# Kernel optimization log

Hardware: AMD Instinct MI355X
Metric: run time of the kernel (lower is better)

## Reference

```python
import jax, jax.numpy as jnp
import numpy as np

N, E, F_IN, HEADS, OUT_PER_HEAD = 50000, 1600000, 128, 4, 32
NEG_SLOPE = 0.2  # LeakyReLU slope used by standard GATConv


def setup_inputs() -> dict:
    key = jax.random.key(0)
    ks = jax.random.split(key, 7)
    x = jax.random.normal(ks[0], (N, F_IN), dtype=jnp.float32)
    edge_src = jax.random.randint(ks[1], (E,), 0, N, dtype=jnp.int64)
    edge_dst = jax.random.randint(ks[2], (E,), 0, N, dtype=jnp.int64)
    W = jax.random.normal(ks[3], (F_IN, HEADS * OUT_PER_HEAD), dtype=jnp.float32) / np.float32(np.sqrt(F_IN))
    a_src = jax.random.normal(ks[4], (HEADS, OUT_PER_HEAD), dtype=jnp.float32) * 0.1
    a_dst = jax.random.normal(ks[5], (HEADS, OUT_PER_HEAD), dtype=jnp.float32) * 0.1
    bias = jnp.zeros((HEADS * OUT_PER_HEAD,), dtype=jnp.float32)
    return {"x": x, "W": W, "a_src": a_src, "a_dst": a_dst, "bias": bias,
            "edge_src": edge_src, "edge_dst": edge_dst}


def reference(x, W, a_src, a_dst, bias, edge_src, edge_dst):
    # GATConv with concat=True over a static edge list (the faithful
    # static-shape form of tf.where(adj>0.5) -> gather -> GAT -> scatter).
    n = x.shape[0]
    H, D = a_src.shape
    h = (x @ W).reshape(n, H, D)                      # [N,H,D] projected features
    # per-node attention logits for source / destination roles
    e_s = jnp.einsum('nhd,hd->nh', h, a_src)          # [N,H]
    e_d = jnp.einsum('nhd,hd->nh', h, a_dst)          # [N,H]
    # per-edge logits with LeakyReLU
    e = jax.nn.leaky_relu(e_s[edge_src] + e_d[edge_dst], NEG_SLOPE)  # [E,H]
    # numerically stable softmax over incoming edges of each destination node
    m = jax.ops.segment_max(e, edge_dst, num_segments=n)             # [N,H]
    m = jnp.where(jnp.isfinite(m), m, 0.0)
    alpha = jnp.exp(e - m[edge_dst])                                 # [E,H]
    denom = jax.ops.segment_sum(alpha, edge_dst, num_segments=n)     # [N,H]
    alpha = alpha / jnp.where(denom > 0, denom, 1.0)[edge_dst]
    # weighted aggregation of source features onto destinations
    msgs = alpha[:, :, None] * h[edge_src]                           # [E,H,D]
    out = jax.ops.segment_sum(msgs, edge_dst, num_segments=n)        # [N,H,D]
    return out.reshape(n, H * D) + bias
```

## Files before the change

kernel.cpp:

```cpp
#include <hip/hip_runtime.h>
#include <math.h>

#define NEG_SLOPE 0.2f
#define NB1 256
#define XROW 136
#define BSHIFT 5
#define BNODES 32
#define CAP 2048

typedef __attribute__((ext_vector_type(8))) short short8;
typedef __attribute__((ext_vector_type(4))) float floatx4;

__device__ __forceinline__ unsigned short f2bf(float f) {
    unsigned int u = __float_as_uint(f);
    u += 0x7fffu + ((u >> 16) & 1u);
    return (unsigned short)(u >> 16);
}
__device__ __forceinline__ float bf2f(unsigned short b) {
    return __uint_as_float(((unsigned int)b) << 16);
}
__device__ __forceinline__ float u2fl(unsigned int u) {
    return __uint_as_float(u << 16);
}
__device__ __forceinline__ float u2fh(unsigned int u) {
    return __uint_as_float(u & 0xffff0000u);
}

__device__ __forceinline__ void fma8(float* a, int o, float wt, const uint4& hv) {
    a[o + 0] = fmaf(wt, u2fl(hv.x), a[o + 0]);
    a[o + 1] = fmaf(wt, u2fh(hv.x), a[o + 1]);
    a[o + 2] = fmaf(wt, u2fl(hv.y), a[o + 2]);
    a[o + 3] = fmaf(wt, u2fh(hv.y), a[o + 3]);
    a[o + 4] = fmaf(wt, u2fl(hv.z), a[o + 4]);
    a[o + 5] = fmaf(wt, u2fh(hv.z), a[o + 5]);
    a[o + 6] = fmaf(wt, u2fl(hv.w), a[o + 6]);
    a[o + 7] = fmaf(wt, u2fh(hv.w), a[o + 7]);
}

__global__ __launch_bounds__(256) void prep_w_kernel(
    const float* __restrict__ W, unsigned short* __restrict__ WThi,
    unsigned short* __restrict__ WTlo, int* __restrict__ gcur, int nbuck)
{
    const int idx = blockIdx.x * 256 + threadIdx.x;
    const int j = idx >> 7, k = idx & 127;
    const float w = W[k * 128 + j];
    const unsigned short hi = f2bf(w);
    const unsigned short lo = f2bf(w - bf2f(hi));
    WThi[idx] = hi;
    WTlo[idx] = lo;
    if (idx < nbuck) gcur[idx] = idx * CAP;
}

__global__ __launch_bounds__(256) void mfma_gemm_kernel(
    const float* __restrict__ x, const unsigned short* __restrict__ WThi,
    const unsigned short* __restrict__ WTlo, const float* __restrict__ a_src,
    const float* __restrict__ a_dst, unsigned short* __restrict__ hb,
    float* __restrict__ es, float* __restrict__ ed, int n)
{
    __shared__ unsigned short Xhi[32 * XROW];
    __shared__ unsigned short Xlo[32 * XROW];
    const int t = threadIdx.x;
    const int wv = t >> 6, lane = t & 63;
    const int l16 = lane & 15, quad = lane >> 4;
    const int node_base = blockIdx.x * 32;

    short8 bh[4][2], bl[4][2];
    #pragma unroll
    for (int c = 0; c < 4; ++c) {
        #pragma unroll
        for (int u = 0; u < 2; ++u) {
            const int j = (wv * 2 + u) * 16 + l16;
            const int ko = c * 32 + quad * 8;
            bh[c][u] = *(const short8*)&WThi[j * 128 + ko];
            bl[c][u] = *(const short8*)&WTlo[j * 128 + ko];
        }
    }

    for (int i = t; i < 1024; i += 256) {
        const int nd = i >> 5;
        const int k4 = i & 31;
        float4 xv = make_float4(0.f, 0.f, 0.f, 0.f);
        if (node_base + nd < n)
            xv = ((const float4*)(x + (size_t)(node_base + nd) * 128))[k4];
        const unsigned short h0 = f2bf(xv.x), h1 = f2bf(xv.y),
                             h2 = f2bf(xv.z), h3 = f2bf(xv.w);
        const unsigned short l0 = f2bf(xv.x - bf2f(h0)), l1 = f2bf(xv.y - bf2f(h1)),
                             l2 = f2bf(xv.z - bf2f(h2)), l3 = f2bf(xv.w - bf2f(h3));
        *(ushort4*)&Xhi[nd * XROW + k4 * 4] = make_ushort4(h0, h1, h2, h3);
        *(ushort4*)&Xlo[nd * XROW + k4 * 4] = make_ushort4(l0, l1, l2, l3);
    }
    __syncthreads();

    floatx4 acc[2][2] = {};
    #pragma unroll
    for (int c = 0; c < 4; ++c) {
        const int ko = c * 32 + quad * 8;
        short8 ah[2], al[2];
        #pragma unroll
        for (int r = 0; r < 2; ++r) {
            ah[r] = *(const short8*)&Xhi[(r * 16 + l16) * XROW + ko];
            al[r] = *(const short8*)&Xlo[(r * 16 + l16) * XROW + ko];
        }
        #pragma unroll
        for (int r = 0; r < 2; ++r)
        #pragma unroll
        for (int u = 0; u < 2; ++u) {
            acc[r][u] = __builtin_amdgcn_mfma_f32_16x16x32_bf16(ah[r], bl[c][u], acc[r][u], 0, 0, 0);
            acc[r][u] = __builtin_amdgcn_mfma_f32_16x16x32_bf16(al[r], bh[c][u], acc[r][u], 0, 0, 0);
            acc[r][u] = __builtin_amdgcn_mfma_f32_16x16x32_bf16(ah[r], bh[c][u], acc[r][u], 0, 0, 0);
        }
    }

    float asv[2], adv[2];
    #pragma unroll
    for (int u = 0; u < 2; ++u) {
        const int feat = (wv * 2 + u) * 16 + l16;
        asv[u] = a_src[feat];
        adv[u] = a_dst[feat];
    }
    #pragma unroll
    for (int r = 0; r < 2; ++r) {
        #pragma unroll
        for (int u = 0; u < 2; ++u) {
            const int feat = (wv * 2 + u) * 16 + l16;
            #pragma unroll
            for (int g = 0; g < 4; ++g) {
                const int node = node_base + r * 16 + quad * 4 + g;
                if (node < n)
                    hb[(size_t)node * 128 + feat] = f2bf(acc[r][u][g]);
            }
        }
        #pragma unroll
        for (int g = 0; g < 4; ++g) {
            float ps = acc[r][0][g] * asv[0] + acc[r][1][g] * asv[1];
            float pd = acc[r][0][g] * adv[0] + acc[r][1][g] * adv[1];
            #pragma unroll
            for (int o = 8; o >= 1; o >>= 1) {
                ps += __shfl_xor(ps, o);
                pd += __shfl_xor(pd, o);
            }
            const int node = node_base + r * 16 + quad * 4 + g;
            if (l16 == 0 && node < n) {
                es[node * 4 + wv] = ps;
                ed[node * 4 + wv] = pd;
            }
        }
    }
}

__global__ __launch_bounds__(256) void bucket_scatter(
    const int* __restrict__ src, const int* __restrict__ dst,
    int* __restrict__ gcur, int* __restrict__ ebuf, int e, int nbuck)
{
    __shared__ unsigned int stash[6272];
    __shared__ int cnt[1600];
    __shared__ int cur[1600];
    const int t = threadIdx.x;
    for (int b = t; b < nbuck; b += 256) cnt[b] = 0;
    __syncthreads();
    const int per = (e + NB1 - 1) / NB1;
    const int lo = blockIdx.x * per;
    const int m = min(e, lo + per) - lo;
    for (int j = t; j < m; j += 256) {
        const int d = dst[lo + j];
        const unsigned int v = (unsigned int)src[lo + j]
                             | ((unsigned int)(d & (BNODES - 1)) << 16)
                             | ((unsigned int)(d >> BSHIFT) << 21);
        stash[j] = v;
        atomicAdd(&cnt[d >> BSHIFT], 1);
    }
    __syncthreads();
    for (int b = t; b < nbuck; b += 256) {
        const int c = cnt[b];
        if (c > 0) cur[b] = atomicAdd(&gcur[b], c);
    }
    __syncthreads();
    for (int j = t; j < m; j += 256) {
        const unsigned int v = stash[j];
        const int pos = atomicAdd(&cur[v >> 21], 1);
        ebuf[pos] = (int)(v & 0x1FFFFFu);
    }
}

__global__ __launch_bounds__(256) void sort_agg_kernel(
    const unsigned short* __restrict__ hb, const float* __restrict__ es,
    const float* __restrict__ ed, const float* __restrict__ bias,
    const int* __restrict__ gcur, const int* __restrict__ ebuf,
    float* __restrict__ out, int n)
{
    __shared__ unsigned short esort[CAP];
    __shared__ int hist[BNODES], hexcl[BNODES], cur[BNODES];
    const int b = blockIdx.x;
    const int t = threadIdx.x;
    const int lane = t & 63;
    const int wv = t >> 6;
    const int l8 = lane & 7;
    const int oct = lane >> 3;
    const int f0 = l8 * 16;
    const int hh = l8 >> 1;

    const int start = b * CAP;
    const int end = gcur[b];

    if (t < BNODES) hist[t] = 0;
    __syncthreads();
    for (int i = start + t; i < end; i += 256)
        atomicAdd(&hist[(ebuf[i] >> 16) & (BNODES - 1)], 1);
    __syncthreads();
    if (wv == 0) {
        const int v = (lane < BNODES) ? hist[lane] : 0;
        int incl = v;
        #pragma unroll
        for (int o = 1; o < BNODES; o <<= 1) {
            const int tt = __shfl_up(incl, o);
            if (lane >= o) incl += tt;
        }
        if (lane < BNODES) { hexcl[lane] = incl - v; cur[lane] = incl - v; }
    }
    __syncthreads();
    for (int i = start + t; i < end; i += 256) {
        const int v = ebuf[i];
        const int pos = atomicAdd(&cur[(v >> 16) & (BNODES - 1)], 1);
        esort[pos] = (unsigned short)(v & 0xFFFF);
    }
    __syncthreads();

    for (int j = 0; j < 8; ++j) {
        const int nd = wv * 8 + j;
        const int node = b * BNODES + nd;
        if (node >= n) break;
        const int off = hexcl[nd];
        const int deg = hist[nd];
        const float edh = ed[(size_t)node * 4 + hh];

        float a[16];
        #pragma unroll
        for (int k = 0; k < 16; ++k) a[k] = 0.f;
        float wsum = 0.f;

        for (int c0 = 0; c0 < deg; c0 += 16) {
            const int ci0 = c0 + oct;
            const int ci1 = ci0 + 8;
            const int dm = deg - 1;
            const int s0 = esort[off + min(ci0, dm)];
            const int s1 = esort[off + min(ci1, dm)];
            const float e0 = es[(size_t)s0 * 4 + hh];
            const float e1 = es[(size_t)s1 * 4 + hh];
            const uint4 hA0 = *(const uint4*)&hb[(size_t)s0 * 128 + f0];
            const uint4 hB0 = *(const uint4*)&hb[(size_t)s0 * 128 + f0 + 8];
            const uint4 hA1 = *(const uint4*)&hb[(size_t)s1 * 128 + f0];
            const uint4 hB1 = *(const uint4*)&hb[(size_t)s1 * 128 + f0 + 8];
            float lg0 = e0 + edh; lg0 = lg0 > 0.f ? lg0 : NEG_SLOPE * lg0;
            float lg1 = e1 + edh; lg1 = lg1 > 0.f ? lg1 : NEG_SLOPE * lg1;
            const float w0 = (ci0 < deg) ? __expf(lg0) : 0.f;
            const float w1 = (ci1 < deg) ? __expf(lg1) : 0.f;
            fma8(a, 0, w0, hA0); fma8(a, 8, w0, hB0);
            fma8(a, 0, w1, hA1); fma8(a, 8, w1, hB1);
            wsum += w0 + w1;
        }
        #pragma unroll
        for (int o = 8; o <= 32; o <<= 1) {
            #pragma unroll
            for (int k = 0; k < 16; ++k) a[k] += __shfl_xor(a[k], o);
            wsum += __shfl_xor(wsum, o);
        }
        if (oct == 0) {
            const float inv = 1.f / ((wsum > 0.f) ? wsum : 1.f);
            #pragma unroll
            for (int q = 0; q < 4; ++q) {
                const float4 bq = *(const float4*)(bias + f0 + q * 4);
                float4 o4;
                o4.x = a[q * 4 + 0] * inv + bq.x;
                o4.y = a[q * 4 + 1] * inv + bq.y;
                o4.z = a[q * 4 + 2] * inv + bq.z;
                o4.w = a[q * 4 + 3] * inv + bq.w;
                *(float4*)(out + (size_t)node * 128 + f0 + q * 4) = o4;
            }
        }
    }
}

extern "C" void kernel_launch(void* const* d_in, const int* in_sizes, int n_in,
                              void* d_out, int out_size, void* d_ws, size_t ws_size,
                              hipStream_t stream)
{
    const float* x      = (const float*)d_in[0];
    const float* W      = (const float*)d_in[1];
    const float* a_src  = (const float*)d_in[2];
    const float* a_dst  = (const float*)d_in[3];
    const float* bias   = (const float*)d_in[4];
    const int*   e_src  = (const int*)d_in[5];
    const int*   e_dst  = (const int*)d_in[6];
    float* out = (float*)d_out;

    const int n = in_sizes[0] / 128;
    const int e = in_sizes[5];
    const int nbuck = (n + BNODES - 1) >> BSHIFT;

    char* ws = (char*)d_ws;
    size_t o = 0;
    auto alloc = [&](size_t bytes) { void* p = ws + o; o += (bytes + 255) & ~(size_t)255; return p; };
    unsigned short* hb   = (unsigned short*)alloc((size_t)n * 128 * sizeof(unsigned short));
    unsigned short* WThi = (unsigned short*)alloc(128 * 128 * sizeof(unsigned short));
    unsigned short* WTlo = (unsigned short*)alloc(128 * 128 * sizeof(unsigned short));
    float* es      = (float*)alloc((size_t)n * 4 * sizeof(float));
    float* ed      = (float*)alloc((size_t)n * 4 * sizeof(float));
    int* gcur      = (int*)alloc((size_t)nbuck * sizeof(int));
    int* ebuf      = (int*)alloc((size_t)nbuck * CAP * sizeof(int));
    (void)ws_size; (void)n_in; (void)out_size;

    prep_w_kernel<<<64, 256, 0, stream>>>(W, WThi, WTlo, gcur, nbuck);
    mfma_gemm_kernel<<<(n + 31) / 32, 256, 0, stream>>>(x, WThi, WTlo, a_src, a_dst,
                                                        hb, es, ed, n);
    bucket_scatter<<<NB1, 256, 0, stream>>>(e_src, e_dst, gcur, ebuf, e, nbuck);
    sort_agg_kernel<<<nbuck, 256, 0, stream>>>(hb, es, ed, bias, gcur, ebuf, out, n);
}
```

Before: 197.3 us.

## Use coarse 128-node buckets in scatter and unroll aggregation loop by 32

The edge bucketing pass now groups edges by 128-node coarse buckets, giving about 391 buckets instead of about 1563. This reduces per-block global atomics and makes ebuf writes less scattered. Each aggregation block then reads its whole coarse bucket and keeps only the quarter that belongs to its 32 fine nodes, so every coarse bucket is read four times. The gather loop is also unrolled to four edges per octet to put more memory loads in flight, at the cost of more registers and extra wasted lanes on low-degree nodes.

```diff
diff --git a/kernel.cpp b/kernel.cpp
--- a/kernel.cpp
+++ b/kernel.cpp
@@ -4,9 +4,11 @@
 #define NEG_SLOPE 0.2f
 #define NB1 256
 #define XROW 136
-#define BSHIFT 5
-#define BNODES 32
-#define CAP 2048
+#define CSHIFT 7
+#define CNODES 128
+#define CAP 4608
+#define FNODES 32
+#define FCAP 2048
 
 typedef __attribute__((ext_vector_type(8))) short short8;
 typedef __attribute__((ext_vector_type(4))) float floatx4;
@@ -39,7 +41,7 @@
 
 __global__ __launch_bounds__(256) void prep_w_kernel(
     const float* __restrict__ W, unsigned short* __restrict__ WThi,
-    unsigned short* __restrict__ WTlo, int* __restrict__ gcur, int nbuck)
+    unsigned short* __restrict__ WTlo, int* __restrict__ gcur, int ncoarse)
 {
     const int idx = blockIdx.x * 256 + threadIdx.x;
     const int j = idx >> 7, k = idx & 127;
@@ -48,7 +50,7 @@
     const unsigned short lo = f2bf(w - bf2f(hi));
     WThi[idx] = hi;
     WTlo[idx] = lo;
-    if (idx < nbuck) gcur[idx] = idx * CAP;
+    if (idx < ncoarse) gcur[idx] = idx * CAP;
 }
 
 __global__ __launch_bounds__(256) void mfma_gemm_kernel(
@@ -150,13 +152,13 @@
 
 __global__ __launch_bounds__(256) void bucket_scatter(
     const int* __restrict__ src, const int* __restrict__ dst,
-    int* __restrict__ gcur, int* __restrict__ ebuf, int e, int nbuck)
+    int* __restrict__ gcur, int* __restrict__ ebuf, int e, int ncoarse)
 {
     __shared__ unsigned int stash[6272];
-    __shared__ int cnt[1600];
-    __shared__ int cur[1600];
+    __shared__ int cnt[392];
+    __shared__ int cur[392];
     const int t = threadIdx.x;
-    for (int b = t; b < nbuck; b += 256) cnt[b] = 0;
+    for (int b = t; b < ncoarse; b += 256) cnt[b] = 0;
     __syncthreads();
     const int per = (e + NB1 - 1) / NB1;
     const int lo = blockIdx.x * per;
@@ -164,21 +166,21 @@
     for (int j = t; j < m; j += 256) {
         const int d = dst[lo + j];
         const unsigned int v = (unsigned int)src[lo + j]
-                             | ((unsigned int)(d & (BNODES - 1)) << 16)
-                             | ((unsigned int)(d >> BSHIFT) << 21);
+                             | ((unsigned int)(d & (CNODES - 1)) << 16)
+                             | ((unsigned int)(d >> CSHIFT) << 23);
         stash[j] = v;
-        atomicAdd(&cnt[d >> BSHIFT], 1);
-    }
-    __syncthreads();
-    for (int b = t; b < nbuck; b += 256) {
+        atomicAdd(&cnt[d >> CSHIFT], 1);
+    }
+    __syncthreads();
+    for (int b = t; b < ncoarse; b += 256) {
         const int c = cnt[b];
         if (c > 0) cur[b] = atomicAdd(&gcur[b], c);
     }
     __syncthreads();
     for (int j = t; j < m; j += 256) {
         const unsigned int v = stash[j];
-        const int pos = atomicAdd(&cur[v >> 21], 1);
-        ebuf[pos] = (int)(v & 0x1FFFFFu);
+        const int pos = atomicAdd(&cur[v >> 23], 1);
+        ebuf[pos] = (int)(v & 0x7FFFFFu);
     }
 }
 
@@ -188,9 +190,11 @@
     const int* __restrict__ gcur, const int* __restrict__ ebuf,
     float* __restrict__ out, int n)
 {
-    __shared__ unsigned short esort[CAP];
-    __shared__ int hist[BNODES], hexcl[BNODES], cur[BNODES];
+    __shared__ unsigned short esort[FCAP];
+    __shared__ int hist[FNODES], hexcl[FNODES], cur[FNODES];
     const int b = blockIdx.x;
+    const int cb = b >> 2;
+    const int q = b & 3;
     const int t = threadIdx.x;
     const int lane = t & 63;
     const int wv = t >> 6;
@@ -199,35 +203,40 @@
     const int f0 = l8 * 16;
     const int hh = l8 >> 1;
 
-    const int start = b * CAP;
-    const int end = gcur[b];
-
-    if (t < BNODES) hist[t] = 0;
-    __syncthreads();
-    for (int i = start + t; i < end; i += 256)
-        atomicAdd(&hist[(ebuf[i] >> 16) & (BNODES - 1)], 1);
+    const int start = cb * CAP;
+    const int end = min(gcur[cb], start + CAP);
+
+    if (t < FNODES) hist[t] = 0;
+    __syncthreads();
+    for (int i = start + t; i < end; i += 256) {
+        const int ld7 = (ebuf[i] >> 16) & (CNODES - 1);
+        if ((ld7 >> 5) == q) atomicAdd(&hist[ld7 & (FNODES - 1)], 1);
+    }
     __syncthreads();
     if (wv == 0) {
-        const int v = (lane < BNODES) ? hist[lane] : 0;
+        const int v = (lane < FNODES) ? hist[lane] : 0;
         int incl = v;
         #pragma unroll
-        for (int o = 1; o < BNODES; o <<= 1) {
+        for (int o = 1; o < FNODES; o <<= 1) {
             const int tt = __shfl_up(incl, o);
             if (lane >= o) incl += tt;
         }
-        if (lane < BNODES) { hexcl[lane] = incl - v; cur[lane] = incl - v; }
+        if (lane < FNODES) { hexcl[lane] = incl - v; cur[lane] = incl - v; }
     }
     __syncthreads();
     for (int i = start + t; i < end; i += 256) {
         const int v = ebuf[i];
-        const int pos = atomicAdd(&cur[(v >> 16) & (BNODES - 1)], 1);
-        esort[pos] = (unsigned short)(v & 0xFFFF);
+        const int ld7 = (v >> 16) & (CNODES - 1);
+        if ((ld7 >> 5) == q) {
+            const int pos = atomicAdd(&cur[ld7 & (FNODES - 1)], 1);
+            esort[pos] = (unsigned short)(v & 0xFFFF);
+        }
     }
     __syncthreads();
 
     for (int j = 0; j < 8; ++j) {
         const int nd = wv * 8 + j;
-        const int node = b * BNODES + nd;
+        const int node = b * FNODES + nd;
         if (node >= n) break;
         const int off = hexcl[nd];
         const int deg = hist[nd];
@@ -238,25 +247,41 @@
         for (int k = 0; k < 16; ++k) a[k] = 0.f;
         float wsum = 0.f;
 
-        for (int c0 = 0; c0 < deg; c0 += 16) {
+        for (int c0 = 0; c0 < deg; c0 += 32) {
+            const int dm = deg - 1;
             const int ci0 = c0 + oct;
             const int ci1 = ci0 + 8;
-            const int dm = deg - 1;
+            const int ci2 = ci0 + 16;
+            const int ci3 = ci0 + 24;
             const int s0 = esort[off + min(ci0, dm)];
             const int s1 = esort[off + min(ci1, dm)];
+            const int s2 = esort[off + min(ci2, dm)];
+            const int s3 = esort[off + min(ci3, dm)];
             const float e0 = es[(size_t)s0 * 4 + hh];
             const float e1 = es[(size_t)s1 * 4 + hh];
+            const float e2 = es[(size_t)s2 * 4 + hh];
+            const float e3 = es[(size_t)s3 * 4 + hh];
             const uint4 hA0 = *(const uint4*)&hb[(size_t)s0 * 128 + f0];
             const uint4 hB0 = *(const uint4*)&hb[(size_t)s0 * 128 + f0 + 8];
             const uint4 hA1 = *(const uint4*)&hb[(size_t)s1 * 128 + f0];
             const uint4 hB1 = *(const uint4*)&hb[(size_t)s1 * 128 + f0 + 8];
+            const uint4 hA2 = *(const uint4*)&hb[(size_t)s2 * 128 + f0];
+            const uint4 hB2 = *(const uint4*)&hb[(size_t)s2 * 128 + f0 + 8];
+            const uint4 hA3 = *(const uint4*)&hb[(size_t)s3 * 128 + f0];
+            const uint4 hB3 = *(const uint4*)&hb[(size_t)s3 * 128 + f0 + 8];
             float lg0 = e0 + edh; lg0 = lg0 > 0.f ? lg0 : NEG_SLOPE * lg0;
             float lg1 = e1 + edh; lg1 = lg1 > 0.f ? lg1 : NEG_SLOPE * lg1;
+            float lg2 = e2 + edh; lg2 = lg2 > 0.f ? lg2 : NEG_SLOPE * lg2;
+            float lg3 = e3 + edh; lg3 = lg3 > 0.f ? lg3 : NEG_SLOPE * lg3;
             const float w0 = (ci0 < deg) ? __expf(lg0) : 0.f;
             const float w1 = (ci1 < deg) ? __expf(lg1) : 0.f;
+            const float w2 = (ci2 < deg) ? __expf(lg2) : 0.f;
+            const float w3 = (ci3 < deg) ? __expf(lg3) : 0.f;
             fma8(a, 0, w0, hA0); fma8(a, 8, w0, hB0);
             fma8(a, 0, w1, hA1); fma8(a, 8, w1, hB1);
-            wsum += w0 + w1;
+            fma8(a, 0, w2, hA2); fma8(a, 8, w2, hB2);
+            fma8(a, 0, w3, hA3); fma8(a, 8, w3, hB3);
+            wsum += (w0 + w1) + (w2 + w3);
         }
         #pragma unroll
         for (int o = 8; o <= 32; o <<= 1) {
@@ -267,14 +292,14 @@
         if (oct == 0) {
             const float inv = 1.f / ((wsum > 0.f) ? wsum : 1.f);
             #pragma unroll
-            for (int q = 0; q < 4; ++q) {
-                const float4 bq = *(const float4*)(bias + f0 + q * 4);
+            for (int qq = 0; qq < 4; ++qq) {
+                const float4 bq = *(const float4*)(bias + f0 + qq * 4);
                 float4 o4;
-                o4.x = a[q * 4 + 0] * inv + bq.x;
-                o4.y = a[q * 4 + 1] * inv + bq.y;
-                o4.z = a[q * 4 + 2] * inv + bq.z;
-                o4.w = a[q * 4 + 3] * inv + bq.w;
-                *(float4*)(out + (size_t)node * 128 + f0 + q * 4) = o4;
+                o4.x = a[qq * 4 + 0] * inv + bq.x;
+                o4.y = a[qq * 4 + 1] * inv + bq.y;
+                o4.z = a[qq * 4 + 2] * inv + bq.z;
+                o4.w = a[qq * 4 + 3] * inv + bq.w;
+                *(float4*)(out + (size_t)node * 128 + f0 + qq * 4) = o4;
             }
         }
     }
@@ -295,7 +320,8 @@
 
     const int n = in_sizes[0] / 128;
     const int e = in_sizes[5];
-    const int nbuck = (n + BNODES - 1) >> BSHIFT;
+    const int ncoarse = (n + CNODES - 1) >> CSHIFT;
+    const int nfine = (n + FNODES - 1) / FNODES;
 
     char* ws = (char*)d_ws;
     size_t o = 0;
@@ -305,13 +331,13 @@
     unsigned short* WTlo = (unsigned short*)alloc(128 * 128 * sizeof(unsigned short));
     float* es      = (float*)alloc((size_t)n * 4 * sizeof(float));
     float* ed      = (float*)alloc((size_t)n * 4 * sizeof(float));
-    int* gcur      = (int*)alloc((size_t)nbuck * sizeof(int));
-    int* ebuf      = (int*)alloc((size_t)nbuck * CAP * sizeof(int));
+    int* gcur      = (int*)alloc((size_t)ncoarse * sizeof(int));
+    int* ebuf      = (int*)alloc((size_t)ncoarse * CAP * sizeof(int));
     (void)ws_size; (void)n_in; (void)out_size;
 
-    prep_w_kernel<<<64, 256, 0, stream>>>(W, WThi, WTlo, gcur, nbuck);
+    prep_w_kernel<<<64, 256, 0, stream>>>(W, WThi, WTlo, gcur, ncoarse);
     mfma_gemm_kernel<<<(n + 31) / 32, 256, 0, stream>>>(x, WThi, WTlo, a_src, a_dst,
                                                         hb, es, ed, n);
-    bucket_scatter<<<NB1, 256, 0, stream>>>(e_src, e_dst, gcur, ebuf, e, nbuck);
-    sort_agg_kernel<<<nbuck, 256, 0, stream>>>(hb, es, ed, bias, gcur, ebuf, out, n);
-}
+    bucket_scatter<<<NB1, 256, 0, stream>>>(e_src, e_dst, gcur, ebuf, e, ncoarse);
+    sort_agg_kernel<<<nfine, 256, 0, stream>>>(hb, es, ed, bias, gcur, ebuf, out, n);
+}
```

Measured after the change: 206.5 us. 4.6% more time.
